# Kernel tuning notes

Hardware: AMD Instinct MI355X
Metric: run time of the kernel (lower is better)

## Reference

```python
import jax, jax.numpy as jnp
import numpy as np

N = 50000      # nodes
E = 800000     # edges
F_IN = 128     # input_channels
H = 128        # hidden_channels
OUT = 10       # output_channels
G = 64         # graphs in batch


def setup_inputs() -> dict:
    key = jax.random.key(0)
    ks = jax.random.split(key, 16)
    s = 0.05
    inp = {
        "x": jax.random.normal(ks[0], (N, F_IN), jnp.float32),
        "edge_index": jax.random.randint(ks[1], (2, E), 0, N, jnp.int64 if jax.config.jax_enable_x64 else jnp.int32),
        "batch": jnp.sort(jax.random.randint(ks[2], (N,), 0, G, jnp.int32)),
        "conv1_w": jax.random.normal(ks[3], (F_IN, H), jnp.float32) * s,
        "conv1_b": jnp.zeros((H,), jnp.float32),
        "conv2_w": jax.random.normal(ks[4], (H, H), jnp.float32) * s,
        "conv2_b": jnp.zeros((H,), jnp.float32),
        "conv3_w": jax.random.normal(ks[5], (H, H), jnp.float32) * s,
        "conv3_b": jnp.zeros((H,), jnp.float32),
        "fc1_w": jax.random.normal(ks[6], (H, 8 * H), jnp.float32) * s,
        "fc1_b": jnp.zeros((8 * H,), jnp.float32),
        "fc2_w": jax.random.normal(ks[7], (8 * H, 4 * H), jnp.float32) * s,
        "fc2_b": jnp.zeros((4 * H,), jnp.float32),
        "fc3_w": jax.random.normal(ks[8], (4 * H, 2 * H), jnp.float32) * s,
        "fc3_b": jnp.zeros((2 * H,), jnp.float32),
        "fc4_w": jax.random.normal(ks[9], (2 * H, H), jnp.float32) * s,
        "fc4_b": jnp.zeros((H,), jnp.float32),
        "fc5_w": jax.random.normal(ks[10], (H, OUT), jnp.float32) * s,
        "fc5_b": jnp.zeros((OUT,), jnp.float32),
    }
    return inp


def _gcn_conv(x, w, b, src, dst, norm, n_nodes):
    # GCNConv: out = D^{-1/2} (A + I) D^{-1/2} X W + b   (self-loops already in src/dst)
    xw = x @ w                                        # [N, H]
    msg = xw[src] * norm[:, None]                     # gather + scale, [E+N, H]
    return jax.ops.segment_sum(msg, dst, num_segments=n_nodes) + b


def reference(x, edge_index, batch,
              conv1_w, conv1_b, conv2_w, conv2_b, conv3_w, conv3_b,
              fc1_w, fc1_b, fc2_w, fc2_b, fc3_w, fc3_b,
              fc4_w, fc4_b, fc5_w, fc5_b):
    n = x.shape[0]
    loop = jnp.arange(n, dtype=edge_index.dtype)
    src = jnp.concatenate([edge_index[0], loop])      # add self-loops
    dst = jnp.concatenate([edge_index[1], loop])
    deg = jax.ops.segment_sum(jnp.ones_like(dst, dtype=x.dtype), dst, num_segments=n)
    dinv = jnp.where(deg > 0, jax.lax.rsqrt(deg), 0.0)
    norm = dinv[src] * dinv[dst]                      # symmetric normalization per edge

    h = jax.nn.relu(_gcn_conv(x, conv1_w, conv1_b, src, dst, norm, n))
    h = jax.nn.relu(_gcn_conv(h, conv2_w, conv2_b, src, dst, norm, n))
    h = _gcn_conv(h, conv3_w, conv3_b, src, dst, norm, n)

    # global mean pool over graphs
    sums = jax.ops.segment_sum(h, batch, num_segments=G)
    cnt = jax.ops.segment_sum(jnp.ones((n,), x.dtype), batch, num_segments=G)
    f = sums / jnp.maximum(cnt, 1.0)[:, None]         # [G, H]

    y = jax.nn.relu(f @ fc1_w + fc1_b)
    y = jax.nn.relu(y @ fc2_w + fc2_b)
    y = jax.nn.relu(y @ fc3_w + fc3_b)
    y = jax.nn.relu(y @ fc4_w + fc4_b)
    # dropout p=0.5 is identity in eval mode
    y = y @ fc5_w + fc5_b                             # [G, OUT]
    return (f, y)
```

## Files before the change

kernel.cpp:

```cpp
#include <hip/hip_runtime.h>
#include <stdint.h>

#define N_NODES 50000
#define N_EDGES 800000
#define FEAT    128
#define NGRAPH  64

#define E_BLKS      3125
#define GSTRIP_BLKS 782
#define GR_BLKS     (GSTRIP_BLKS + E_BLKS)

typedef __attribute__((ext_vector_type(8))) short short8;
typedef __attribute__((ext_vector_type(4))) float floatx4;

static __device__ __forceinline__ ushort f2bf(float f) {
  uint32_t x = __float_as_uint(f);
  x += 0x7FFF + ((x >> 16) & 1);
  return (ushort)(x >> 16);
}
static __device__ __forceinline__ float bfLo(uint32_t u) {
  return __uint_as_float(u << 16);
}
static __device__ __forceinline__ float bfHi(uint32_t u) {
  return __uint_as_float(u & 0xFFFF0000u);
}

static __device__ __forceinline__ void cvt4T(const float* __restrict__ in,
                                             ushort* __restrict__ outT, int i) {
  float4 v = ((const float4*)in)[i];
  int k = (4 * i) >> 7;
  int n = (4 * i) & 127;
  outT[(size_t)(n + 0) * FEAT + k] = f2bf(v.x);
  outT[(size_t)(n + 1) * FEAT + k] = f2bf(v.y);
  outT[(size_t)(n + 2) * FEAT + k] = f2bf(v.z);
  outT[(size_t)(n + 3) * FEAT + k] = f2bf(v.w);
}

__global__ __launch_bounds__(256) void wcvt(const float* __restrict__ w0,
                                            const float* __restrict__ w1,
                                            ushort* __restrict__ wbT) {
  int i = blockIdx.x * 256 + threadIdx.x;
  if (i < 4096) cvt4T(w0, wbT, i);
  else cvt4T(w1, wbT + FEAT * FEAT, i - 4096);
}

static __device__ __forceinline__ void gemm_strip_f32a(int strip, int lane,
                                                       const float* __restrict__ X,
                                                       const ushort* __restrict__ WT,
                                                       ushort* __restrict__ XW) {
  if (strip >= N_NODES / 16) return;
  int m0 = strip * 16;
  int r = lane & 15, quad = lane >> 4;
  const float* xrow = X + (size_t)(m0 + r) * FEAT;
  short8 afr[4];
#pragma unroll
  for (int kb = 0; kb < 4; ++kb) {
    int k0 = kb * 32 + quad * 8;
    float4 f0 = *(const float4*)(xrow + k0);
    float4 f1 = *(const float4*)(xrow + k0 + 4);
    short8 a;
    a[0] = (short)f2bf(f0.x); a[1] = (short)f2bf(f0.y);
    a[2] = (short)f2bf(f0.z); a[3] = (short)f2bf(f0.w);
    a[4] = (short)f2bf(f1.x); a[5] = (short)f2bf(f1.y);
    a[6] = (short)f2bf(f1.z); a[7] = (short)f2bf(f1.w);
    afr[kb] = a;
  }
#pragma unroll
  for (int nt = 0; nt < 8; ++nt) {
    int n0 = nt * 16;
    floatx4 acc = {0.f, 0.f, 0.f, 0.f};
    const ushort* wrow = WT + (size_t)(n0 + r) * FEAT;
#pragma unroll
    for (int kb = 0; kb < 4; ++kb) {
      short8 b = *(const short8*)(wrow + kb * 32 + quad * 8);
      acc = __builtin_amdgcn_mfma_f32_16x16x32_bf16(afr[kb], b, acc, 0, 0, 0);
    }
#pragma unroll
    for (int reg = 0; reg < 4; ++reg)
      XW[(size_t)(m0 + quad * 4 + reg) * FEAT + n0 + r] = f2bf(acc[reg]);
  }
}

__global__ __launch_bounds__(256) void gemm_rank(const float* __restrict__ x,
                                                 const ushort* __restrict__ wbT,
                                                 ushort* __restrict__ msl,
                                                 const int* __restrict__ dst,
                                                 int* __restrict__ cnt_p,
                                                 int* __restrict__ rank) {
  int b = blockIdx.x, t = threadIdx.x;
  int fifth = b / 5;
  if (b - fifth * 5 == 0) {
    gemm_strip_f32a(fifth * 4 + (t >> 6), t & 63, x, wbT, msl);
  } else {
    int e = (b - fifth - 1) * 256 + t;
    rank[e] = atomicAdd(&cnt_p[dst[e] * 8], 1);
  }
}

__global__ __launch_bounds__(256) void gemm2_strip(const ushort* __restrict__ X,
                                                   const ushort* __restrict__ WT,
                                                   ushort* __restrict__ XW) {
  int strip = (blockIdx.x * 256 + threadIdx.x) >> 6;
  int lane = threadIdx.x & 63;
  if (strip >= N_NODES / 16) return;
  int m0 = strip * 16;
  int r = lane & 15, quad = lane >> 4;
  const ushort* xrow = X + (size_t)(m0 + r) * FEAT;
  short8 afr[4];
#pragma unroll
  for (int kb = 0; kb < 4; ++kb)
    afr[kb] = *(const short8*)(xrow + kb * 32 + quad * 8);
#pragma unroll
  for (int nt = 0; nt < 8; ++nt) {
    int n0 = nt * 16;
    floatx4 acc = {0.f, 0.f, 0.f, 0.f};
    const ushort* wrow = WT + (size_t)(n0 + r) * FEAT;
#pragma unroll
    for (int kb = 0; kb < 4; ++kb) {
      short8 b = *(const short8*)(wrow + kb * 32 + quad * 8);
      acc = __builtin_amdgcn_mfma_f32_16x16x32_bf16(afr[kb], b, acc, 0, 0, 0);
    }
#pragma unroll
    for (int reg = 0; reg < 4; ++reg)
      XW[(size_t)(m0 + quad * 4 + reg) * FEAT + n0 + r] = f2bf(acc[reg]);
  }
}

__global__ __launch_bounds__(256) void dinv_scan1(const int* __restrict__ cnt_p,
                                                  const int* __restrict__ batch,
                                                  float* __restrict__ dinv,
                                                  float* __restrict__ cnt_g,
                                                  int* __restrict__ ptr,
                                                  int* __restrict__ bsums) {
  __shared__ int tmp[256];
  __shared__ int bins[NGRAPH];
  if (threadIdx.x < NGRAPH) bins[threadIdx.x] = 0;
  int i = blockIdx.x * 256 + threadIdx.x;
  int v = (i < N_NODES) ? cnt_p[i * 8] : 0;
  tmp[threadIdx.x] = v;
  __syncthreads();
  for (int off = 1; off < 256; off <<= 1) {
    int t = (threadIdx.x >= off) ? tmp[threadIdx.x - off] : 0;
    __syncthreads();
    tmp[threadIdx.x] += t;
    __syncthreads();
  }
  if (i < N_NODES) ptr[i] = tmp[threadIdx.x] - v;
  if (threadIdx.x == 255) bsums[blockIdx.x] = tmp[255];
  if (i < N_NODES) {
    dinv[i] = rsqrtf((float)v + 1.0f);
    atomicAdd(&bins[batch[i]], 1);
  }
  __syncthreads();
  if (threadIdx.x < NGRAPH && bins[threadIdx.x] > 0)
    atomicAdd(&cnt_g[threadIdx.x], (float)bins[threadIdx.x]);
}

__global__ __launch_bounds__(256) void scan2(int* __restrict__ bsums, int nb) {
  __shared__ int tmp[256];
  int v = (threadIdx.x < nb) ? bsums[threadIdx.x] : 0;
  tmp[threadIdx.x] = v;
  __syncthreads();
  for (int off = 1; off < 256; off <<= 1) {
    int t = (threadIdx.x >= off) ? tmp[threadIdx.x - off] : 0;
    __syncthreads();
    tmp[threadIdx.x] += t;
    __syncthreads();
  }
  if (threadIdx.x < nb) bsums[threadIdx.x] = tmp[threadIdx.x] - v;
}

__global__ __launch_bounds__(256) void scan3(int* __restrict__ ptr,
                                             const int* __restrict__ bsums) {
  int i = blockIdx.x * 256 + threadIdx.x;
  if (i < N_NODES) ptr[i] += bsums[blockIdx.x];
}

__global__ __launch_bounds__(256) void fill_csr(const int* __restrict__ src,
                                                const int* __restrict__ dst,
                                                const int* __restrict__ rank,
                                                const int* __restrict__ ptr,
                                                const float* __restrict__ dinv,
                                                int2* __restrict__ edges) {
  int e = blockIdx.x * 256 + threadIdx.x;
  if (e >= N_EDGES) return;
  int s = src[e];
  edges[ptr[dst[e]] + rank[e]] = make_int2(s, __float_as_int(dinv[s]));
}

static __device__ __forceinline__ float2 agg_node(const uint32_t* __restrict__ m32,
                                                  const int2* __restrict__ edges,
                                                  int start, int n, int lane) {
  float ax0 = 0.f, ay0 = 0.f, ax1 = 0.f, ay1 = 0.f;
  float ax2 = 0.f, ay2 = 0.f, ax3 = 0.f, ay3 = 0.f;
  int i = 0;
  if ((start & 1) && n > 0) {
    int2 e = edges[start];
    uint32_t u = m32[(size_t)e.x * 64 + lane];
    float nrm = __int_as_float(e.y);
    ax0 = fmaf(nrm, bfLo(u), ax0);
    ay0 = fmaf(nrm, bfHi(u), ay0);
    i = 1;
  }
  for (; i + 8 <= n; i += 8) {
    const int4* ep = (const int4*)(edges + start + i);
    int4 q0 = ep[0], q1 = ep[1], q2 = ep[2], q3 = ep[3];
    uint32_t u0 = m32[(size_t)q0.x * 64 + lane];
    uint32_t u1 = m32[(size_t)q0.z * 64 + lane];
    uint32_t u2 = m32[(size_t)q1.x * 64 + lane];
    uint32_t u3 = m32[(size_t)q1.z * 64 + lane];
    uint32_t u4 = m32[(size_t)q2.x * 64 + lane];
    uint32_t u5 = m32[(size_t)q2.z * 64 + lane];
    uint32_t u6 = m32[(size_t)q3.x * 64 + lane];
    uint32_t u7 = m32[(size_t)q3.z * 64 + lane];
    float n0 = __int_as_float(q0.y), n1 = __int_as_float(q0.w);
    float n2 = __int_as_float(q1.y), n3 = __int_as_float(q1.w);
    float n4 = __int_as_float(q2.y), n5 = __int_as_float(q2.w);
    float n6 = __int_as_float(q3.y), n7 = __int_as_float(q3.w);
    ax0 = fmaf(n0, bfLo(u0), ax0); ay0 = fmaf(n0, bfHi(u0), ay0);
    ax1 = fmaf(n1, bfLo(u1), ax1); ay1 = fmaf(n1, bfHi(u1), ay1);
    ax2 = fmaf(n2, bfLo(u2), ax2); ay2 = fmaf(n2, bfHi(u2), ay2);
    ax3 = fmaf(n3, bfLo(u3), ax3); ay3 = fmaf(n3, bfHi(u3), ay3);
    ax0 = fmaf(n4, bfLo(u4), ax0); ay0 = fmaf(n4, bfHi(u4), ay0);
    ax1 = fmaf(n5, bfLo(u5), ax1); ay1 = fmaf(n5, bfHi(u5), ay1);
    ax2 = fmaf(n6, bfLo(u6), ax2); ay2 = fmaf(n6, bfHi(u6), ay2);
    ax3 = fmaf(n7, bfLo(u7), ax3); ay3 = fmaf(n7, bfHi(u7), ay3);
  }
  for (; i < n; ++i) {
    int2 e = edges[start + i];
    float nrm = __int_as_float(e.y);
    uint32_t u = m32[(size_t)e.x * 64 + lane];
    ax0 = fmaf(nrm, bfLo(u), ax0);
    ay0 = fmaf(nrm, bfHi(u), ay0);
  }
  return make_float2((ax0 + ax1) + (ax2 + ax3), (ay0 + ay1) + (ay2 + ay3));
}

template <int MODE>
__global__ __launch_bounds__(256) void agg_kernel(const ushort* __restrict__ msg,
                                                  const float* __restrict__ dinv,
                                                  const int* __restrict__ ptr,
                                                  const int* __restrict__ cnt_p,
                                                  const int2* __restrict__ edges,
                                                  const float* __restrict__ bias,
                                                  void* __restrict__ outp) {
  int wave = (blockIdx.x * 256 + threadIdx.x) >> 6;
  int lane = threadIdx.x & 63;
  if (wave >= N_NODES) return;
  int v = wave;
  float di = dinv[v];
  const uint32_t* m32 = (const uint32_t*)msg;
  uint32_t su = m32[(size_t)v * 64 + lane];
  float2 s = agg_node(m32, edges, ptr[v], cnt_p[v * 8], lane);
  float ax = fmaf(di, bfLo(su), s.x);
  float ay = fmaf(di, bfHi(su), s.y);
  if (MODE == 2) {
    ((float2*)outp)[(size_t)v * 64 + lane] = make_float2(ax * di, ay * di);
  } else {
    ax = fmaf(ax, di, bias[2 * lane]);
    ay = fmaf(ay, di, bias[2 * lane + 1]);
    ushort2 h2;
    h2.x = f2bf(fmaxf(ax, 0.f));
    h2.y = f2bf(fmaxf(ay, 0.f));
    ((ushort2*)outp)[(size_t)v * 64 + lane] = h2;
  }
}

__global__ __launch_bounds__(256) void pool_sum(const float* __restrict__ a3,
                                                const int* __restrict__ batch,
                                                float* __restrict__ P) {
  int wave = blockIdx.x * 4 + (threadIdx.x >> 6);
  int lane = threadIdx.x & 63;
  int v0 = wave * 16;
  if (v0 >= N_NODES) return;
  int vend = v0 + 16;
  if (vend > N_NODES) vend = N_NODES;
  const float2* a2 = (const float2*)a3;
  float ax = 0.f, ay = 0.f;
  int g = batch[v0];
  for (int v = v0; v < vend; ++v) {
    int gv = batch[v];
    if (gv != g) {
      atomicAdd(&P[(size_t)g * FEAT + 2 * lane], ax);
      atomicAdd(&P[(size_t)g * FEAT + 2 * lane + 1], ay);
      ax = 0.f; ay = 0.f; g = gv;
    }
    float2 t = a2[(size_t)v * 64 + lane];
    ax += t.x;
    ay += t.y;
  }
  atomicAdd(&P[(size_t)g * FEAT + 2 * lane], ax);
  atomicAdd(&P[(size_t)g * FEAT + 2 * lane + 1], ay);
}

template <int K, int C, int KSLICE, int RELU_IN, int DIVC, int NSPLIT>
__global__ __launch_bounds__(256) void fc_layer(const float* __restrict__ IN,
                                                const float* __restrict__ W,
                                                const float* __restrict__ Bs,
                                                const float* __restrict__ cntg,
                                                float* __restrict__ OUT) {
  constexpr int CB = (C + 63) / 64;
  int lane = threadIdx.x & 63;
  int gq = threadIdx.x >> 6;
  int bid = blockIdx.x;
  int kp = bid % NSPLIT;
  int rest = bid / NSPLIT;
  int cg = rest % CB;
  int g = (rest / CB) * 4 + gq;
  int c = cg * 64 + lane;
  if (c >= C) return;
  int k0 = kp * KSLICE;
  const float* wp = W + (size_t)k0 * C + c;
  const float* in = IN + (size_t)g * K + k0;
  float cf = 1.f;
  if (DIVC) cf = fmaxf(cntg[g], 1.f);
  float a0 = 0.f, a1 = 0.f, a2 = 0.f, a3 = 0.f;
  float a4 = 0.f, a5 = 0.f, a6 = 0.f, a7 = 0.f;
#pragma unroll 2
  for (int k = 0; k < KSLICE; k += 8) {
    float i0 = in[k + 0], i1 = in[k + 1], i2 = in[k + 2], i3 = in[k + 3];
    float i4 = in[k + 4], i5 = in[k + 5], i6 = in[k + 6], i7 = in[k + 7];
    if (RELU_IN) {
      i0 = fmaxf(i0, 0.f); i1 = fmaxf(i1, 0.f);
      i2 = fmaxf(i2, 0.f); i3 = fmaxf(i3, 0.f);
      i4 = fmaxf(i4, 0.f); i5 = fmaxf(i5, 0.f);
      i6 = fmaxf(i6, 0.f); i7 = fmaxf(i7, 0.f);
    }
    if (DIVC) {
      i0 /= cf; i1 /= cf; i2 /= cf; i3 /= cf;
      i4 /= cf; i5 /= cf; i6 /= cf; i7 /= cf;
    }
    a0 = fmaf(i0, wp[(size_t)(k + 0) * C], a0);
    a1 = fmaf(i1, wp[(size_t)(k + 1) * C], a1);
    a2 = fmaf(i2, wp[(size_t)(k + 2) * C], a2);
    a3 = fmaf(i3, wp[(size_t)(k + 3) * C], a3);
    a4 = fmaf(i4, wp[(size_t)(k + 4) * C], a4);
    a5 = fmaf(i5, wp[(size_t)(k + 5) * C], a5);
    a6 = fmaf(i6, wp[(size_t)(k + 6) * C], a6);
    a7 = fmaf(i7, wp[(size_t)(k + 7) * C], a7);
  }
  float s = ((a0 + a1) + (a2 + a3)) + ((a4 + a5) + (a6 + a7));
  if (NSPLIT == 1) {
    OUT[(size_t)g * C + c] = s + Bs[c];
  } else {
    atomicAdd(&OUT[(size_t)g * C + c], s + (kp == 0 ? Bs[c] : 0.f));
  }
}

extern "C" void kernel_launch(void* const* d_in, const int* in_sizes, int n_in,
                              void* d_out, int out_size, void* d_ws, size_t ws_size,
                              hipStream_t stream) {
  const float* x         = (const float*)d_in[0];
  const int*   ei        = (const int*)d_in[1];
  const int*   batch     = (const int*)d_in[2];
  const float* conv_w[3] = {(const float*)d_in[3], (const float*)d_in[5], (const float*)d_in[7]};
  const float* conv_b[3] = {(const float*)d_in[4], (const float*)d_in[6], (const float*)d_in[8]};
  const float* fc_w[5]   = {(const float*)d_in[9],  (const float*)d_in[11],
                            (const float*)d_in[13], (const float*)d_in[15],
                            (const float*)d_in[17]};
  const float* fc_b[5]   = {(const float*)d_in[10], (const float*)d_in[12],
                            (const float*)d_in[14], (const float*)d_in[16],
                            (const float*)d_in[18]};
  const int* e_src = ei;
  const int* e_dst = ei + N_EDGES;
  float* out_f = (float*)d_out;
  float* out_y = (float*)d_out + NGRAPH * FEAT;

  char* p = (char*)d_ws;
  auto carve = [&](size_t bytes) {
    char* r = p;
    p += (bytes + 255) & ~(size_t)255;
    return r;
  };
  int*    cnt_p   = (int*)carve((size_t)N_NODES * 32);
  float*  dinv    = (float*)carve(N_NODES * 4);
  int*    csr_ptr = (int*)carve(N_NODES * 4);
  int*    bsums   = (int*)carve(256 * 4);
  int2*   edges   = (int2*)carve((size_t)N_EDGES * 8);
  ushort* wbT     = (ushort*)carve((size_t)2 * FEAT * FEAT * 2);
  ushort* hbuf    = (ushort*)carve((size_t)N_NODES * FEAT * 2);
  float*  f_sum   = (float*)carve(NGRAPH * FEAT * 4);
  float*  cnt_g   = (float*)carve(NGRAPH * 4);
  float*  Y1      = (float*)carve(NGRAPH * 1024 * 4);
  float*  Y2      = (float*)carve(NGRAPH * 512 * 4);
  float*  Y3      = (float*)carve(NGRAPH * 256 * 4);
  float*  Y4      = (float*)carve(NGRAPH * 128 * 4);
  char*   region  = carve((size_t)N_EDGES * 4 + 2 * (size_t)N_NODES * FEAT * 2);
  int*    rank    = (int*)region;
  ushort* msl1    = (ushort*)(region + (size_t)N_EDGES * 4);
  ushort* msl2    = (ushort*)(region + (size_t)N_EDGES * 4 + (size_t)N_NODES * FEAT * 2);
  float*  a3      = (float*)region;

  const int BLK_N = (N_NODES + 255) / 256;

  hipMemsetAsync(cnt_p, 0, (size_t)N_NODES * 32, stream);
  hipMemsetAsync(f_sum, 0, NGRAPH * FEAT * 4 + 256, stream);
  hipMemsetAsync(Y2, 0, NGRAPH * (512 + 256 + 128) * 4, stream);

  wcvt<<<32, 256, 0, stream>>>(conv_w[0], conv_w[1], wbT);

  gemm_rank<<<GR_BLKS, 256, 0, stream>>>(x, wbT, msl1, e_dst, cnt_p, rank);

  dinv_scan1<<<BLK_N, 256, 0, stream>>>(cnt_p, batch, dinv, cnt_g, csr_ptr, bsums);
  scan2<<<1, 256, 0, stream>>>(bsums, BLK_N);
  scan3<<<BLK_N, 256, 0, stream>>>(csr_ptr, bsums);

  fill_csr<<<E_BLKS, 256, 0, stream>>>(e_src, e_dst, rank, csr_ptr, dinv, edges);

  const int AGG_BLKS  = (N_NODES + 3) / 4;
  const int POOL_BLKS = (N_NODES / 16 + 3) / 4 + 1;

  agg_kernel<0><<<AGG_BLKS, 256, 0, stream>>>(msl1, dinv, csr_ptr, cnt_p, edges,
                                              conv_b[0], hbuf);
  gemm2_strip<<<GSTRIP_BLKS, 256, 0, stream>>>(hbuf, wbT + FEAT * FEAT, msl2);
  agg_kernel<0><<<AGG_BLKS, 256, 0, stream>>>(msl2, dinv, csr_ptr, cnt_p, edges,
                                              conv_b[1], hbuf);
  agg_kernel<2><<<AGG_BLKS, 256, 0, stream>>>(hbuf, dinv, csr_ptr, cnt_p, edges,
                                              nullptr, a3);
  pool_sum<<<POOL_BLKS, 256, 0, stream>>>(a3, batch, f_sum);

  fc_layer< 128, 128, 128, 0, 1, 1><<< 32, 256, 0, stream>>>(f_sum, conv_w[2], conv_b[2], cnt_g, out_f);
  fc_layer< 128,1024, 128, 0, 0, 1><<<256, 256, 0, stream>>>(out_f, fc_w[0], fc_b[0], nullptr, Y1);
  fc_layer<1024, 512, 256, 1, 0, 4><<<512, 256, 0, stream>>>(Y1, fc_w[1], fc_b[1], nullptr, Y2);
  fc_layer< 512, 256, 128, 1, 0, 4><<<256, 256, 0, stream>>>(Y2, fc_w[2], fc_b[2], nullptr, Y3);
  fc_layer< 256, 128,  32, 1, 0, 8><<<256, 256, 0, stream>>>(Y3, fc_w[3], fc_b[3], nullptr, Y4);
  fc_layer< 128,  10, 128, 1, 0, 1><<< 16, 256, 0, stream>>>(Y4, fc_w[4], fc_b[4], nullptr, out_y);
}
```

Measured before the change: 366.3 us.

## Fold third GCN aggregation and mean pool into per-graph coefficient matrix GEMM

Drops the third message-passing pass and the separate pooling kernel. Pooling is linear, so it builds a dense per-graph coefficient matrix coefT[G][N] from self-loop terms (dinv²) and scattered edge terms (dinv[s]*dinv[d]) while the CSR is filled. The pooled sums then come from a single MFMA GEMM over the layer-2 activations. This removes a full edge gather over 128 features plus an fp32 intermediate, at the cost of a 12.8 MB zero-fill, 800k extra float atomics in fill_csr, and bf16 rounding of the coefficients.

```diff
diff --git a/kernel.cpp b/kernel.cpp
--- a/kernel.cpp
+++ b/kernel.cpp
@@ -3,12 +3,16 @@
 
 #define N_NODES 50000
 #define N_EDGES 800000
+#define N_PAD   50176
+#define PCHUNK  512
+#define NCHUNKS 98
 #define FEAT    128
 #define NGRAPH  64
 
 #define E_BLKS      3125
 #define GSTRIP_BLKS 782
 #define GR_BLKS     (GSTRIP_BLKS + E_BLKS)
+#define CZ_BLKS     3136
 
 typedef __attribute__((ext_vector_type(8))) short short8;
 typedef __attribute__((ext_vector_type(4))) float floatx4;
@@ -86,14 +90,20 @@
                                                  ushort* __restrict__ msl,
                                                  const int* __restrict__ dst,
                                                  int* __restrict__ cnt_p,
-                                                 int* __restrict__ rank) {
+                                                 int* __restrict__ rank,
+                                                 float* __restrict__ coefT) {
   int b = blockIdx.x, t = threadIdx.x;
-  int fifth = b / 5;
-  if (b - fifth * 5 == 0) {
-    gemm_strip_f32a(fifth * 4 + (t >> 6), t & 63, x, wbT, msl);
+  if (b < GR_BLKS) {
+    int fifth = b / 5;
+    if (b - fifth * 5 == 0) {
+      gemm_strip_f32a(fifth * 4 + (t >> 6), t & 63, x, wbT, msl);
+    } else {
+      int e = (b - fifth - 1) * 256 + t;
+      rank[e] = atomicAdd(&cnt_p[dst[e] * 8], 1);
+    }
   } else {
-    int e = (b - fifth - 1) * 256 + t;
-    rank[e] = atomicAdd(&cnt_p[dst[e] * 8], 1);
+    int i = (b - GR_BLKS) * 256 + t;
+    ((float4*)coefT)[i] = make_float4(0.f, 0.f, 0.f, 0.f);
   }
 }
 
@@ -131,7 +141,8 @@
                                                   float* __restrict__ dinv,
                                                   float* __restrict__ cnt_g,
                                                   int* __restrict__ ptr,
-                                                  int* __restrict__ bsums) {
+                                                  int* __restrict__ bsums,
+                                                  float* __restrict__ coefT) {
   __shared__ int tmp[256];
   __shared__ int bins[NGRAPH];
   if (threadIdx.x < NGRAPH) bins[threadIdx.x] = 0;
@@ -148,8 +159,11 @@
   if (i < N_NODES) ptr[i] = tmp[threadIdx.x] - v;
   if (threadIdx.x == 255) bsums[blockIdx.x] = tmp[255];
   if (i < N_NODES) {
-    dinv[i] = rsqrtf((float)v + 1.0f);
-    atomicAdd(&bins[batch[i]], 1);
+    float di = rsqrtf((float)v + 1.0f);
+    dinv[i] = di;
+    int g = batch[i];
+    coefT[(size_t)g * N_PAD + i] = di * di;
+    atomicAdd(&bins[g], 1);
   }
   __syncthreads();
   if (threadIdx.x < NGRAPH && bins[threadIdx.x] > 0)
@@ -181,11 +195,16 @@
                                                 const int* __restrict__ rank,
                                                 const int* __restrict__ ptr,
                                                 const float* __restrict__ dinv,
-                                                int2* __restrict__ edges) {
+                                                const int* __restrict__ batch,
+                                                int2* __restrict__ edges,
+                                                float* __restrict__ coefT) {
   int e = blockIdx.x * 256 + threadIdx.x;
   if (e >= N_EDGES) return;
   int s = src[e];
-  edges[ptr[dst[e]] + rank[e]] = make_int2(s, __float_as_int(dinv[s]));
+  int d = dst[e];
+  float ds = dinv[s];
+  edges[ptr[d] + rank[e]] = make_int2(s, __float_as_int(ds));
+  atomicAdd(&coefT[(size_t)batch[d] * N_PAD + s], ds * dinv[d]);
 }
 
 static __device__ __forceinline__ float2 agg_node(const uint32_t* __restrict__ m32,
@@ -236,14 +255,13 @@
   return make_float2((ax0 + ax1) + (ax2 + ax3), (ay0 + ay1) + (ay2 + ay3));
 }
 
-template <int MODE>
 __global__ __launch_bounds__(256) void agg_kernel(const ushort* __restrict__ msg,
                                                   const float* __restrict__ dinv,
                                                   const int* __restrict__ ptr,
                                                   const int* __restrict__ cnt_p,
                                                   const int2* __restrict__ edges,
                                                   const float* __restrict__ bias,
-                                                  void* __restrict__ outp) {
+                                                  ushort* __restrict__ outp) {
   int wave = (blockIdx.x * 256 + threadIdx.x) >> 6;
   int lane = threadIdx.x & 63;
   if (wave >= N_NODES) return;
@@ -252,45 +270,64 @@
   const uint32_t* m32 = (const uint32_t*)msg;
   uint32_t su = m32[(size_t)v * 64 + lane];
   float2 s = agg_node(m32, edges, ptr[v], cnt_p[v * 8], lane);
-  float ax = fmaf(di, bfLo(su), s.x);
-  float ay = fmaf(di, bfHi(su), s.y);
-  if (MODE == 2) {
-    ((float2*)outp)[(size_t)v * 64 + lane] = make_float2(ax * di, ay * di);
-  } else {
-    ax = fmaf(ax, di, bias[2 * lane]);
-    ay = fmaf(ay, di, bias[2 * lane + 1]);
-    ushort2 h2;
-    h2.x = f2bf(fmaxf(ax, 0.f));
-    h2.y = f2bf(fmaxf(ay, 0.f));
-    ((ushort2*)outp)[(size_t)v * 64 + lane] = h2;
-  }
-}
-
-__global__ __launch_bounds__(256) void pool_sum(const float* __restrict__ a3,
-                                                const int* __restrict__ batch,
-                                                float* __restrict__ P) {
-  int wave = blockIdx.x * 4 + (threadIdx.x >> 6);
-  int lane = threadIdx.x & 63;
-  int v0 = wave * 16;
-  if (v0 >= N_NODES) return;
-  int vend = v0 + 16;
-  if (vend > N_NODES) vend = N_NODES;
-  const float2* a2 = (const float2*)a3;
-  float ax = 0.f, ay = 0.f;
-  int g = batch[v0];
-  for (int v = v0; v < vend; ++v) {
-    int gv = batch[v];
-    if (gv != g) {
-      atomicAdd(&P[(size_t)g * FEAT + 2 * lane], ax);
-      atomicAdd(&P[(size_t)g * FEAT + 2 * lane + 1], ay);
-      ax = 0.f; ay = 0.f; g = gv;
-    }
-    float2 t = a2[(size_t)v * 64 + lane];
-    ax += t.x;
-    ay += t.y;
-  }
-  atomicAdd(&P[(size_t)g * FEAT + 2 * lane], ax);
-  atomicAdd(&P[(size_t)g * FEAT + 2 * lane + 1], ay);
+  float ax = fmaf(fmaf(di, bfLo(su), s.x), di, bias[2 * lane]);
+  float ay = fmaf(fmaf(di, bfHi(su), s.y), di, bias[2 * lane + 1]);
+  ushort2 h2;
+  h2.x = f2bf(fmaxf(ax, 0.f));
+  h2.y = f2bf(fmaxf(ay, 0.f));
+  ((ushort2*)outp)[(size_t)v * 64 + lane] = h2;
+}
+
+__global__ __launch_bounds__(512) void pool_mfma(const ushort* __restrict__ h2,
+                                                 const float* __restrict__ coefT,
+                                                 float* __restrict__ P) {
+  __shared__ ushort cs[64 * PCHUNK];
+  int t = threadIdx.x;
+  int lane = t & 63;
+  int w = t >> 6;
+  int r = lane & 15, quad = lane >> 4;
+  int n0 = w * 16;
+  floatx4 acc[4];
+#pragma unroll
+  for (int mt = 0; mt < 4; ++mt) acc[mt] = (floatx4){0.f, 0.f, 0.f, 0.f};
+#pragma unroll 1
+  for (int cc = 0; cc < 2; ++cc) {
+    int c0 = (blockIdx.x * 2 + cc) * PCHUNK;
+#pragma unroll 4
+    for (int it = 0; it < 16; ++it) {
+      int f4 = t + it * 512;
+      int g = f4 >> 7;
+      int k = (f4 & 127) * 4;
+      float4 v = *(const float4*)(coefT + (size_t)g * N_PAD + c0 + k);
+      ushort4 u;
+      u.x = f2bf(v.x); u.y = f2bf(v.y); u.z = f2bf(v.z); u.w = f2bf(v.w);
+      uint32_t off = ((uint32_t)g * (PCHUNK * 2) + k * 2) ^ ((g & 7) << 4);
+      *(ushort4*)((char*)cs + off) = u;
+    }
+    __syncthreads();
+#pragma unroll 2
+    for (int kb = 0; kb < 16; ++kb) {
+      int k0c = kb * 32 + quad * 8;
+      short8 bfr;
+#pragma unroll
+      for (int j = 0; j < 8; ++j)
+        bfr[j] = (short)h2[(size_t)(c0 + k0c + j) * FEAT + n0 + r];
+#pragma unroll
+      for (int mt = 0; mt < 4; ++mt) {
+        int row = mt * 16 + r;
+        uint32_t off = ((uint32_t)row * (PCHUNK * 2) + k0c * 2) ^ ((row & 7) << 4);
+        short8 a = *(const short8*)((const char*)cs + off);
+        acc[mt] = __builtin_amdgcn_mfma_f32_16x16x32_bf16(a, bfr, acc[mt], 0, 0, 0);
+      }
+    }
+    __syncthreads();
+  }
+#pragma unroll
+  for (int mt = 0; mt < 4; ++mt)
+#pragma unroll
+    for (int reg = 0; reg < 4; ++reg)
+      atomicAdd(&P[(size_t)(mt * 16 + quad * 4 + reg) * FEAT + n0 + r],
+                acc[mt][reg]);
 }
 
 template <int K, int C, int KSLICE, int RELU_IN, int DIVC, int NSPLIT>
@@ -378,18 +415,18 @@
   int*    bsums   = (int*)carve(256 * 4);
   int2*   edges   = (int2*)carve((size_t)N_EDGES * 8);
   ushort* wbT     = (ushort*)carve((size_t)2 * FEAT * FEAT * 2);
-  ushort* hbuf    = (ushort*)carve((size_t)N_NODES * FEAT * 2);
+  ushort* hbuf    = (ushort*)carve((size_t)N_PAD * FEAT * 2);
+  float*  coefT   = (float*)carve((size_t)NGRAPH * N_PAD * 4);
   float*  f_sum   = (float*)carve(NGRAPH * FEAT * 4);
   float*  cnt_g   = (float*)carve(NGRAPH * 4);
   float*  Y1      = (float*)carve(NGRAPH * 1024 * 4);
   float*  Y2      = (float*)carve(NGRAPH * 512 * 4);
   float*  Y3      = (float*)carve(NGRAPH * 256 * 4);
   float*  Y4      = (float*)carve(NGRAPH * 128 * 4);
-  char*   region  = carve((size_t)N_EDGES * 4 + 2 * (size_t)N_NODES * FEAT * 2);
+  char*   region  = carve((size_t)N_EDGES * 4 + (size_t)N_NODES * FEAT * 2);
   int*    rank    = (int*)region;
   ushort* msl1    = (ushort*)(region + (size_t)N_EDGES * 4);
-  ushort* msl2    = (ushort*)(region + (size_t)N_EDGES * 4 + (size_t)N_NODES * FEAT * 2);
-  float*  a3      = (float*)region;
+  ushort* msl2    = (ushort*)region;
 
   const int BLK_N = (N_NODES + 255) / 256;
 
@@ -399,25 +436,25 @@
 
   wcvt<<<32, 256, 0, stream>>>(conv_w[0], conv_w[1], wbT);
 
-  gemm_rank<<<GR_BLKS, 256, 0, stream>>>(x, wbT, msl1, e_dst, cnt_p, rank);
-
-  dinv_scan1<<<BLK_N, 256, 0, stream>>>(cnt_p, batch, dinv, cnt_g, csr_ptr, bsums);
+  gemm_rank<<<GR_BLKS + CZ_BLKS, 256, 0, stream>>>(x, wbT, msl1, e_dst, cnt_p,
+                                                   rank, coefT);
+
+  dinv_scan1<<<BLK_N, 256, 0, stream>>>(cnt_p, batch, dinv, cnt_g, csr_ptr,
+                                        bsums, coefT);
   scan2<<<1, 256, 0, stream>>>(bsums, BLK_N);
   scan3<<<BLK_N, 256, 0, stream>>>(csr_ptr, bsums);
 
-  fill_csr<<<E_BLKS, 256, 0, stream>>>(e_src, e_dst, rank, csr_ptr, dinv, edges);
-
-  const int AGG_BLKS  = (N_NODES + 3) / 4;
-  const int POOL_BLKS = (N_NODES / 16 + 3) / 4 + 1;
-
-  agg_kernel<0><<<AGG_BLKS, 256, 0, stream>>>(msl1, dinv, csr_ptr, cnt_p, edges,
-                                              conv_b[0], hbuf);
+  fill_csr<<<E_BLKS, 256, 0, stream>>>(e_src, e_dst, rank, csr_ptr, dinv,
+                                       batch, edges, coefT);
+
+  const int AGG_BLKS = (N_NODES + 3) / 4;
+
+  agg_kernel<<<AGG_BLKS, 256, 0, stream>>>(msl1, dinv, csr_ptr, cnt_p, edges,
+                                           conv_b[0], hbuf);
   gemm2_strip<<<GSTRIP_BLKS, 256, 0, stream>>>(hbuf, wbT + FEAT * FEAT, msl2);
-  agg_kernel<0><<<AGG_BLKS, 256, 0, stream>>>(msl2, dinv, csr_ptr, cnt_p, edges,
-                                              conv_b[1], hbuf);
-  agg_kernel<2><<<AGG_BLKS, 256, 0, stream>>>(hbuf, dinv, csr_ptr, cnt_p, edges,
-                                              nullptr, a3);
-  pool_sum<<<POOL_BLKS, 256, 0, stream>>>(a3, batch, f_sum);
+  agg_kernel<<<AGG_BLKS, 256, 0, stream>>>(msl2, dinv, csr_ptr, cnt_p, edges,
+                                           conv_b[1], hbuf);
+  pool_mfma<<<NCHUNKS / 2, 512, 0, stream>>>(hbuf, coefT, f_sum);
 
   fc_layer< 128, 128, 128, 0, 1, 1><<< 32, 256, 0, stream>>>(f_sum, conv_w[2], conv_b[2], cnt_g, out_f);
   fc_layer< 128,1024, 128, 0, 0, 1><<<256, 256, 0, stream>>>(out_f, fc_w[0], fc_b[0], nullptr, Y1);
```

Result: no change. 364.7 us (-0.4%).
